# Performance work log

Measured on AMD Instinct MI355X. Metric: run time of the kernel, lower is better.

Reference implementation:

```python
import jax, jax.numpy as jnp
import numpy as np

HID = 16   # hidden_dim
K = 16     # kNN neighbors
B = 64     # graphs per batch
N_TS = 8192
N_LC = 12288


def setup_inputs() -> dict:
    key = jax.random.key(0)
    ks = jax.random.split(key, 24)

    def lin(k, fan_in, fan_out):
        w = jax.random.normal(k, (fan_in, fan_out), jnp.float32) / np.sqrt(fan_in).astype(np.float32)
        return w

    inp = {
        "x_ts": jax.random.normal(ks[0], (N_TS, 6), jnp.float32),
        "x_lc": jax.random.normal(ks[1], (N_LC, 5), jnp.float32),
        # balanced sorted graph ids -> every graph has >= K source nodes
        "batch_ts": jnp.repeat(jnp.arange(B, dtype=jnp.int32), N_TS // B),
        "batch_lc": jnp.repeat(jnp.arange(B, dtype=jnp.int32), N_LC // B),
        # ts_encode: Linear(6,16), ELU, Linear(16,16), ELU
        "ts_w1": lin(ks[2], 6, HID),  "ts_b1": jnp.zeros((HID,), jnp.float32),
        "ts_w2": lin(ks[3], HID, HID), "ts_b2": jnp.zeros((HID,), jnp.float32),
        # lc_encode: Linear(5,16), ELU, Linear(16,16), ELU
        "lc_w1": lin(ks[4], 5, HID),  "lc_b1": jnp.zeros((HID,), jnp.float32),
        "lc_w2": lin(ks[5], HID, HID), "lc_b2": jnp.zeros((HID,), jnp.float32),
        # EdgeConv nn: Linear(2*16, 16), ELU  (shared across the 3 conv calls)
        "conv_w": lin(ks[6], 2 * HID, HID), "conv_b": jnp.zeros((HID,), jnp.float32),
        # output MLP 16->64->32->8->4->1 (ELU between, none after last)
        "out_w1": lin(ks[7], HID, 64), "out_b1": jnp.zeros((64,), jnp.float32),
        "out_w2": lin(ks[8], 64, 32),  "out_b2": jnp.zeros((32,), jnp.float32),
        "out_w3": lin(ks[9], 32, 8),   "out_b3": jnp.zeros((8,), jnp.float32),
        "out_w4": lin(ks[10], 8, 4),   "out_b4": jnp.zeros((4,), jnp.float32),
        "out_w5": lin(ks[11], 4, 1),   "out_b5": jnp.zeros((1,), jnp.float32),
    }
    return inp


def _mlp2(x, w1, b1, w2, b2):
    return jax.nn.elu(jax.nn.elu(x @ w1 + b1) @ w2 + b2)


def _edge_conv(x_src, x_dst, b_src, b_dst, w, b):
    """DynamicEdgeConv: per-graph kNN of dst queries into src, message
    nn(cat[x_i, x_j - x_i]), max-aggregate over the K neighbors."""
    # squared distances [N_dst, N_src]
    d2 = (jnp.sum(x_dst * x_dst, 1)[:, None]
          - 2.0 * (x_dst @ x_src.T)
          + jnp.sum(x_src * x_src, 1)[None, :])
    d2 = jnp.where(b_dst[:, None] == b_src[None, :], d2, jnp.inf)
    _, idx = jax.lax.top_k(-d2, K)          # [N_dst, K] nearest (incl. self when src==dst)
    xj = x_src[idx]                          # [N_dst, K, H] gather
    xi = x_dst[:, None, :]                   # [N_dst, 1, H]
    msg = jnp.concatenate([jnp.broadcast_to(xi, xj.shape), xj - xi], axis=-1)
    msg = jax.nn.elu(msg @ w + b)            # [N_dst, K, H]
    return jnp.max(msg, axis=1)              # max aggregation -> [N_dst, H]


def reference(x_ts, x_lc, batch_ts, batch_lc,
              ts_w1, ts_b1, ts_w2, ts_b2,
              lc_w1, lc_b1, lc_w2, lc_b2,
              conv_w, conv_b,
              out_w1, out_b1, out_w2, out_b2, out_w3, out_b3,
              out_w4, out_b4, out_w5, out_b5):
    x_ts_enc = _mlp2(x_ts, ts_w1, ts_b1, ts_w2, ts_b2)   # [N_ts, 16]
    x_lc_enc = _mlp2(x_lc, lc_w1, lc_b1, lc_w2, lc_b2)   # [N_lc, 16]

    feats1 = _edge_conv(x_lc_enc, x_lc_enc, batch_lc, batch_lc, conv_w, conv_b)  # [N_lc,16]
    feats2 = _edge_conv(x_lc_enc, x_ts_enc, batch_lc, batch_ts, conv_w, conv_b)  # [N_ts,16]
    feats3 = _edge_conv(feats1,   feats2,   batch_lc, batch_ts, conv_w, conv_b)  # [N_ts,16]

    # avg_pool_x(batch_ts, feats3, batch_ts): per-graph mean
    sums = jax.ops.segment_sum(feats3, batch_ts, num_segments=B)
    cnts = jax.ops.segment_sum(jnp.ones((feats3.shape[0],), feats3.dtype), batch_ts, num_segments=B)
    pooled = sums / cnts[:, None]                         # [B, 16]

    h = jax.nn.elu(pooled @ out_w1 + out_b1)
    h = jax.nn.elu(h @ out_w2 + out_b2)
    h = jax.nn.elu(h @ out_w3 + out_b3)
    h = jax.nn.elu(h @ out_w4 + out_b4)
    out = h @ out_w5 + out_b5                             # [B, 1]
    batch_out = jnp.arange(B, dtype=batch_ts.dtype)
    return (out, batch_out)
```

## Files before the change

### kernel.cpp

```cpp
#include <hip/hip_runtime.h>
#include <math.h>

#define HID 16
#define KNN 16
#define NB 64
#define NTS 8192
#define NLC 12288
#define TSG 128
#define LCG 192

__device__ __forceinline__ float eluf(float x) {
    return x > 0.0f ? x : expm1f(x);
}

__device__ __forceinline__ unsigned int f2ord(float f) {
    unsigned int b = __float_as_uint(f);
    return b ^ (((int)b >> 31) | 0x80000000u);
}

__global__ __launch_bounds__(256) void encode_kernel(
    const float* __restrict__ x_ts, const float* __restrict__ x_lc,
    const float* __restrict__ ts_w1, const float* __restrict__ ts_b1,
    const float* __restrict__ ts_w2, const float* __restrict__ ts_b2,
    const float* __restrict__ lc_w1, const float* __restrict__ lc_b1,
    const float* __restrict__ lc_w2, const float* __restrict__ lc_b2,
    const float* __restrict__ cw,
    float* __restrict__ ts_enc, float* __restrict__ lc_enc,
    float* __restrict__ y_lc, float* __restrict__ n_lc,
    float* __restrict__ pooled)
{
    __shared__ float sw1[6 * HID];
    __shared__ float sw2[HID * HID];
    __shared__ float scw2[HID * HID];
    __shared__ float sb1[HID];
    __shared__ float sb2[HID];
    __shared__ float s_h[64 * 17];

    const int tid = threadIdx.x;
    const int t = blockIdx.x * 256 + tid;
    if (t < NB * HID) pooled[t] = 0.0f;

    const bool is_ts = (blockIdx.x < NTS / 64);
    const float* w1 = is_ts ? ts_w1 : lc_w1;
    const float* b1 = is_ts ? ts_b1 : lc_b1;
    const float* w2 = is_ts ? ts_w2 : lc_w2;
    const float* b2 = is_ts ? ts_b2 : lc_b2;
    const int in_dim = is_ts ? 6 : 5;

    if (tid < in_dim * HID) sw1[tid] = w1[tid];
    if (tid < HID * HID)    sw2[tid] = w2[tid];
    if (!is_ts && tid < HID * HID) scw2[tid] = cw[HID * HID + tid];
    if (tid < HID)          { sb1[tid] = b1[tid]; sb2[tid] = b2[tid]; }
    __syncthreads();

    const int q    = tid & 3;
    const int rloc = tid >> 2;
    const int row  = is_ts ? (blockIdx.x * 64 + rloc)
                           : ((blockIdx.x - 128) * 64 + rloc);
    const float* x = is_ts ? (x_ts + (size_t)row * 6) : (x_lc + (size_t)row * 5);
    float* outp    = is_ts ? (ts_enc + (size_t)row * HID) : (lc_enc + (size_t)row * HID);

    float xin[6];
    for (int k = 0; k < in_dim; ++k) xin[k] = x[k];

    #pragma unroll
    for (int jc = 0; jc < 4; ++jc) {
        const int c = 4 * q + jc;
        float s = sb1[c];
        for (int k = 0; k < in_dim; ++k) s += xin[k] * sw1[k * HID + c];
        s_h[rloc * 17 + c] = eluf(s);
    }
    __syncthreads();
    float hf[HID];
    #pragma unroll
    for (int k = 0; k < HID; ++k) hf[k] = s_h[rloc * 17 + k];

    float o4v[4];
    #pragma unroll
    for (int jc = 0; jc < 4; ++jc) {
        const int c = 4 * q + jc;
        float s = sb2[c];
        #pragma unroll
        for (int k = 0; k < HID; ++k) s += hf[k] * sw2[k * HID + c];
        o4v[jc] = eluf(s);
    }
    reinterpret_cast<float4*>(outp)[q] = make_float4(o4v[0], o4v[1], o4v[2], o4v[3]);

    if (!is_ts) {
        __syncthreads();
        #pragma unroll
        for (int jc = 0; jc < 4; ++jc) s_h[rloc * 17 + 4 * q + jc] = o4v[jc];
        __syncthreads();
        float of[HID];
        #pragma unroll
        for (int k = 0; k < HID; ++k) of[k] = s_h[rloc * 17 + k];
        float nv = 0.f;
        #pragma unroll
        for (int c = 0; c < HID; ++c) nv += of[c] * of[c];
        float y4[4];
        #pragma unroll
        for (int jc = 0; jc < 4; ++jc) {
            const int c = 4 * q + jc;
            float s = 0.f;
            #pragma unroll
            for (int k = 0; k < HID; ++k) s += of[k] * scw2[k * HID + c];
            y4[jc] = s;
        }
        reinterpret_cast<float4*>(y_lc + (size_t)row * HID)[q] =
            make_float4(y4[0], y4[1], y4[2], y4[3]);
        if (q == 0) n_lc[row] = nv;
    }
}

#define CONV_SMEM_FLOATS (LCG * HID + 2 * HID * HID + 2 * HID)
#define CONV_SMEM_BYTES  (CONV_SMEM_FLOATS * 4)

template<int NSRC, int NDST, bool POOL, bool EPI>
__device__ __forceinline__ void edgeconv_impl(
    float* __restrict__ smem, int bid,
    const float* __restrict__ src, const float* __restrict__ src_y,
    const float* __restrict__ src_n, const float* __restrict__ dst,
    const float* __restrict__ cw, const float* __restrict__ cb,
    float* __restrict__ out_feats, float* __restrict__ out_y,
    float* __restrict__ out_n, float* __restrict__ pool_out)
{
    constexpr int RPB = 8;
    constexpr int BPG = NDST / RPB;
    float* s_y    = smem;
    float* s_dw   = s_y + NSRC * HID;
    float* s_w2   = s_dw + HID * HID;
    float* s_b    = s_w2 + HID * HID;
    float* s_pool = s_b + HID;

    const int tid  = threadIdx.x;
    const int lane = tid & 63;
    const int wave = tid >> 6;
    const int g      = bid / BPG;
    const int rowblk = bid % BPG;

    if (tid < HID * HID) {
        float w1v = cw[tid];
        float w2v = cw[HID * HID + tid];
        s_dw[tid] = w1v - w2v;
        if (EPI) s_w2[tid] = w2v;
    }
    if (tid < HID) s_b[tid] = cb[tid];
    if (POOL && tid < HID) s_pool[tid] = 0.0f;
    {
        const float4* gy = reinterpret_cast<const float4*>(src_y + (size_t)(g * NSRC) * HID);
        float4* sy4 = reinterpret_cast<float4*>(s_y);
        for (int i = tid; i < NSRC * HID / 4; i += 512) sy4[i] = gy[i];
    }

    float rw[3][HID];
    float rn[3];
    #pragma unroll
    for (int k = 0; k < 3; ++k) {
        const float4* rp = reinterpret_cast<const float4*>(src + (size_t)(g * NSRC + lane + 64 * k) * HID);
        float4 a = rp[0], b = rp[1], c4 = rp[2], e = rp[3];
        rw[k][0] = a.x;  rw[k][1] = a.y;  rw[k][2]  = a.z;  rw[k][3]  = a.w;
        rw[k][4] = b.x;  rw[k][5] = b.y;  rw[k][6]  = b.z;  rw[k][7]  = b.w;
        rw[k][8] = c4.x; rw[k][9] = c4.y; rw[k][10] = c4.z; rw[k][11] = c4.w;
        rw[k][12] = e.x; rw[k][13] = e.y; rw[k][14] = e.z;  rw[k][15] = e.w;
        rn[k] = src_n[g * NSRC + lane + 64 * k];
    }

    const int drow = rowblk * RPB + wave;
    const float4* d4 = reinterpret_cast<const float4*>(dst + (size_t)(g * NDST + drow) * HID);
    float xi[HID];
    {
        float4 a = d4[0], b = d4[1], c4 = d4[2], e = d4[3];
        xi[0] = a.x;  xi[1] = a.y;  xi[2]  = a.z;  xi[3]  = a.w;
        xi[4] = b.x;  xi[5] = b.y;  xi[6]  = b.z;  xi[7]  = b.w;
        xi[8] = c4.x; xi[9] = c4.y; xi[10] = c4.z; xi[11] = c4.w;
        xi[12] = e.x; xi[13] = e.y; xi[14] = e.z;  xi[15] = e.w;
    }
    float nd = 0.f;
    #pragma unroll
    for (int c = 0; c < HID; ++c) nd += xi[c] * xi[c];

    unsigned int dk0, dk1, dk2;
    {
        unsigned int dk[3];
        #pragma unroll
        for (int k = 0; k < 3; ++k) {
            float dot = 0.f;
            #pragma unroll
            for (int c = 0; c < HID; ++c) dot += xi[c] * rw[k][c];
            dk[k] = f2ord(nd - 2.0f * dot + rn[k]);
        }
        dk0 = dk[0]; dk1 = dk[1]; dk2 = dk[2];
    }

    unsigned int p = 0;
    int k = KNN;
    for (int b = 31; b >= 0; --b) {
        unsigned int pb = p >> b;
        int cnt = __popcll(__ballot((dk0 >> b) == pb))
                + __popcll(__ballot((dk1 >> b) == pb))
                + __popcll(__ballot((dk2 >> b) == pb));
        if (k > cnt) { k -= cnt; p |= (1u << b); }
    }
    int cnt_eq = __popcll(__ballot(dk0 == p))
               + __popcll(__ballot(dk1 == p))
               + __popcll(__ballot(dk2 == p));
    unsigned int qi = 255u;
    if (cnt_eq != k) {
        qi = 0;
        int kk = k;
        const unsigned int i0 = (unsigned)lane, i1 = (unsigned)(lane + 64), i2 = (unsigned)(lane + 128);
        for (int b = 7; b >= 0; --b) {
            unsigned int qb = qi >> b;
            int cnt = __popcll(__ballot(dk0 == p && (i0 >> b) == qb))
                    + __popcll(__ballot(dk1 == p && (i1 >> b) == qb))
                    + __popcll(__ballot(dk2 == p && (i2 >> b) == qb));
            if (kk > cnt) { kk -= cnt; qi |= (1u << b); }
        }
    }
    unsigned long long m0 = __ballot(dk0 < p || (dk0 == p && (unsigned)lane <= qi));
    unsigned long long m1 = __ballot(dk1 < p || (dk1 == p && (unsigned)(lane + 64) <= qi));
    unsigned long long m2 = __ballot(dk2 < p || (dk2 == p && (unsigned)(lane + 128) <= qi));

    __syncthreads();

    const int c = lane & 15;
    float cic = s_b[c];
    #pragma unroll
    for (int r = 0; r < HID; ++r) cic += xi[r] * s_dw[r * HID + c];

    int jarr[KNN];
    #pragma unroll
    for (int i = 0; i < KNN; ++i) {
        int j;
        if (m0)      { j = __builtin_ctzll(m0);       m0 &= m0 - 1; }
        else if (m1) { j = 64 + __builtin_ctzll(m1);  m1 &= m1 - 1; }
        else         { j = 128 + __builtin_ctzll(m2); m2 &= m2 - 1; }
        jarr[i] = j;
    }
    float yv[KNN];
    #pragma unroll
    for (int i = 0; i < KNN; ++i) yv[i] = s_y[jarr[i] * HID + c];
    float ym = yv[0];
    #pragma unroll
    for (int i = 1; i < KNN; ++i) ym = fmaxf(ym, yv[i]);

    const float f = eluf(cic + ym);

    if (POOL) {
        if (lane < HID) atomicAdd(&s_pool[c], f);
        __syncthreads();
        if (tid < HID) atomicAdd(&pool_out[g * HID + tid], s_pool[tid]);
    } else {
        const int grow = g * NDST + drow;
        if (lane < HID) out_feats[(size_t)grow * HID + c] = f;
        if (EPI) {
            float yvv = 0.f, nv = 0.f;
            #pragma unroll
            for (int r = 0; r < HID; ++r) {
                float fr = __shfl(f, r, 64);
                yvv += fr * s_w2[r * HID + c];
                nv += fr * fr;
            }
            if (lane < HID) out_y[(size_t)grow * HID + c] = yvv;
            if (lane == 0)  out_n[grow] = nv;
        }
    }
}

#define C1_BLOCKS (NB * (LCG / 8))
#define C2_BLOCKS (NB * (TSG / 8))
__global__ __launch_bounds__(512) void edgeconv12_kernel(
    const float* __restrict__ lc_enc, const float* __restrict__ y_lc,
    const float* __restrict__ n_lc, const float* __restrict__ ts_enc,
    const float* __restrict__ cw, const float* __restrict__ cb,
    float* __restrict__ feats1, float* __restrict__ y_f1, float* __restrict__ n_f1,
    float* __restrict__ feats2)
{
    extern __shared__ float smem[];
    if (blockIdx.x < C1_BLOCKS)
        edgeconv_impl<LCG, LCG, false, true>(smem, blockIdx.x, lc_enc, y_lc, n_lc,
                                             lc_enc, cw, cb, feats1, y_f1, n_f1, nullptr);
    else
        edgeconv_impl<LCG, TSG, false, false>(smem, blockIdx.x - C1_BLOCKS, lc_enc, y_lc, n_lc,
                                              ts_enc, cw, cb, feats2, nullptr, nullptr, nullptr);
}

__global__ __launch_bounds__(512) void edgeconv3_kernel(
    const float* __restrict__ feats1, const float* __restrict__ y_f1,
    const float* __restrict__ n_f1, const float* __restrict__ feats2,
    const float* __restrict__ cw, const float* __restrict__ cb,
    float* __restrict__ pooled)
{
    extern __shared__ float smem[];
    edgeconv_impl<LCG, TSG, true, false>(smem, blockIdx.x, feats1, y_f1, n_f1,
                                         feats2, cw, cb, nullptr, nullptr, nullptr, pooled);
}

__global__ __launch_bounds__(64) void head_kernel(
    const float* __restrict__ pooled,
    const float* __restrict__ w1, const float* __restrict__ b1,
    const float* __restrict__ w2, const float* __restrict__ b2,
    const float* __restrict__ w3, const float* __restrict__ b3,
    const float* __restrict__ w4, const float* __restrict__ b4,
    const float* __restrict__ w5, const float* __restrict__ b5,
    float* __restrict__ out)
{
    const int g = blockIdx.x;
    const int lane = threadIdx.x;
    __shared__ float sp[HID];
    __shared__ float sh1[64];
    __shared__ float sh2[32];
    __shared__ float sh3[8];
    __shared__ float sh4[4];

    if (lane < HID) sp[lane] = pooled[g * HID + lane] * (1.0f / (float)TSG);
    __syncthreads();

    {
        float s = b1[lane];
        #pragma unroll
        for (int r = 0; r < HID; ++r) s += sp[r] * w1[r * 64 + lane];
        sh1[lane] = eluf(s);
    }
    __syncthreads();
    if (lane < 32) {
        float s = b2[lane];
        #pragma unroll
        for (int r = 0; r < 64; ++r) s += sh1[r] * w2[r * 32 + lane];
        sh2[lane] = eluf(s);
    }
    __syncthreads();
    if (lane < 8) {
        float s = b3[lane];
        #pragma unroll
        for (int r = 0; r < 32; ++r) s += sh2[r] * w3[r * 8 + lane];
        sh3[lane] = eluf(s);
    }
    __syncthreads();
    if (lane < 4) {
        float s = b4[lane];
        #pragma unroll
        for (int r = 0; r < 8; ++r) s += sh3[r] * w4[r * 4 + lane];
        sh4[lane] = eluf(s);
    }
    __syncthreads();
    if (lane == 0) {
        float s = b5[0];
        #pragma unroll
        for (int r = 0; r < 4; ++r) s += sh4[r] * w5[r];
        out[g] = s;
        out[NB + g] = (float)g;
    }
}

extern "C" void kernel_launch(void* const* d_in, const int* in_sizes, int n_in,
                              void* d_out, int out_size, void* d_ws, size_t ws_size,
                              hipStream_t stream) {
    const float* x_ts  = (const float*)d_in[0];
    const float* x_lc  = (const float*)d_in[1];
    const float* ts_w1 = (const float*)d_in[4];
    const float* ts_b1 = (const float*)d_in[5];
    const float* ts_w2 = (const float*)d_in[6];
    const float* ts_b2 = (const float*)d_in[7];
    const float* lc_w1 = (const float*)d_in[8];
    const float* lc_b1 = (const float*)d_in[9];
    const float* lc_w2 = (const float*)d_in[10];
    const float* lc_b2 = (const float*)d_in[11];
    const float* cw    = (const float*)d_in[12];
    const float* cb    = (const float*)d_in[13];
    const float* ow1   = (const float*)d_in[14];
    const float* ob1   = (const float*)d_in[15];
    const float* ow2   = (const float*)d_in[16];
    const float* ob2   = (const float*)d_in[17];
    const float* ow3   = (const float*)d_in[18];
    const float* ob3   = (const float*)d_in[19];
    const float* ow4   = (const float*)d_in[20];
    const float* ob4   = (const float*)d_in[21];
    const float* ow5   = (const float*)d_in[22];
    const float* ob5   = (const float*)d_in[23];
    float* out = (float*)d_out;

    float* ws = (float*)d_ws;
    float* ts_enc = ws;
    float* lc_enc = ws + 131072;
    float* feats1 = ws + 327680;
    float* feats2 = ws + 524288;
    float* pooled = ws + 655360;
    float* y_lc   = ws + 656384;
    float* n_lc   = ws + 852992;
    float* y_f1   = ws + 865280;
    float* n_f1   = ws + 1061888;

    encode_kernel<<<(NTS + NLC) / 64, 256, 0, stream>>>(
        x_ts, x_lc, ts_w1, ts_b1, ts_w2, ts_b2, lc_w1, lc_b1, lc_w2, lc_b2,
        cw, ts_enc, lc_enc, y_lc, n_lc, pooled);

    edgeconv12_kernel<<<C1_BLOCKS + C2_BLOCKS, 512, CONV_SMEM_BYTES, stream>>>(
        lc_enc, y_lc, n_lc, ts_enc, cw, cb, feats1, y_f1, n_f1, feats2);

    edgeconv3_kernel<<<C2_BLOCKS, 512, CONV_SMEM_BYTES, stream>>>(
        feats1, y_f1, n_f1, feats2, cw, cb, pooled);

    head_kernel<<<NB, 64, 0, stream>>>(
        pooled, ow1, ob1, ow2, ob2, ow3, ob3, ow4, ob4, ow5, ob5, out);
}
```

Measured before the change: 156.6 us.

## Drop shared-memory staging in edgeconv, use wave-independent blocks and 16-bit radix select

Each edge-conv block no longer stages the per-graph y table and the weight matrices in shared memory. Every wave now handles one destination row on its own, reading source rows and y values straight from global memory (cached). The kNN radix select now runs over the upper 16 bits first and only refines the lower 16 bits when there are ties, which cuts the usual number of ballot rounds. The W1-W2 difference is precomputed once in the encode kernel, and the pooling now does one global atomic per wave instead of a shared-memory reduction. These changes remove block-wide syncs and LDS traffic and should raise occupancy, at the cost of redundant global and L2 reads and more global atomics.

Result: slower. 163.6 us (+4.5%).

```diff
diff --git a/kernel.cpp b/kernel.cpp
--- a/kernel.cpp
+++ b/kernel.cpp
@@ -27,7 +27,7 @@
     const float* __restrict__ cw,
     float* __restrict__ ts_enc, float* __restrict__ lc_enc,
     float* __restrict__ y_lc, float* __restrict__ n_lc,
-    float* __restrict__ pooled)
+    float* __restrict__ pooled, float* __restrict__ dw_ws)
 {
     __shared__ float sw1[6 * HID];
     __shared__ float sw2[HID * HID];
@@ -39,6 +39,7 @@
     const int tid = threadIdx.x;
     const int t = blockIdx.x * 256 + tid;
     if (t < NB * HID) pooled[t] = 0.0f;
+    if (blockIdx.x == 0) dw_ws[tid] = cw[tid] - cw[HID * HID + tid];
 
     const bool is_ts = (blockIdx.x < NTS / 64);
     const float* w1 = is_ts ? ts_w1 : lc_w1;
@@ -112,60 +113,20 @@
     }
 }
 
-#define CONV_SMEM_FLOATS (LCG * HID + 2 * HID * HID + 2 * HID)
-#define CONV_SMEM_BYTES  (CONV_SMEM_FLOATS * 4)
-
-template<int NSRC, int NDST, bool POOL, bool EPI>
-__device__ __forceinline__ void edgeconv_impl(
-    float* __restrict__ smem, int bid,
+template<int NSRC, int NDST, int MODE>
+__device__ __forceinline__ void edgeconv_wave(
+    int wid,
     const float* __restrict__ src, const float* __restrict__ src_y,
     const float* __restrict__ src_n, const float* __restrict__ dst,
-    const float* __restrict__ cw, const float* __restrict__ cb,
+    const float* __restrict__ dw, const float* __restrict__ w2,
+    const float* __restrict__ cb,
     float* __restrict__ out_feats, float* __restrict__ out_y,
     float* __restrict__ out_n, float* __restrict__ pool_out)
 {
-    constexpr int RPB = 8;
-    constexpr int BPG = NDST / RPB;
-    float* s_y    = smem;
-    float* s_dw   = s_y + NSRC * HID;
-    float* s_w2   = s_dw + HID * HID;
-    float* s_b    = s_w2 + HID * HID;
-    float* s_pool = s_b + HID;
-
-    const int tid  = threadIdx.x;
-    const int lane = tid & 63;
-    const int wave = tid >> 6;
-    const int g      = bid / BPG;
-    const int rowblk = bid % BPG;
-
-    if (tid < HID * HID) {
-        float w1v = cw[tid];
-        float w2v = cw[HID * HID + tid];
-        s_dw[tid] = w1v - w2v;
-        if (EPI) s_w2[tid] = w2v;
-    }
-    if (tid < HID) s_b[tid] = cb[tid];
-    if (POOL && tid < HID) s_pool[tid] = 0.0f;
-    {
-        const float4* gy = reinterpret_cast<const float4*>(src_y + (size_t)(g * NSRC) * HID);
-        float4* sy4 = reinterpret_cast<float4*>(s_y);
-        for (int i = tid; i < NSRC * HID / 4; i += 512) sy4[i] = gy[i];
-    }
-
-    float rw[3][HID];
-    float rn[3];
-    #pragma unroll
-    for (int k = 0; k < 3; ++k) {
-        const float4* rp = reinterpret_cast<const float4*>(src + (size_t)(g * NSRC + lane + 64 * k) * HID);
-        float4 a = rp[0], b = rp[1], c4 = rp[2], e = rp[3];
-        rw[k][0] = a.x;  rw[k][1] = a.y;  rw[k][2]  = a.z;  rw[k][3]  = a.w;
-        rw[k][4] = b.x;  rw[k][5] = b.y;  rw[k][6]  = b.z;  rw[k][7]  = b.w;
-        rw[k][8] = c4.x; rw[k][9] = c4.y; rw[k][10] = c4.z; rw[k][11] = c4.w;
-        rw[k][12] = e.x; rw[k][13] = e.y; rw[k][14] = e.z;  rw[k][15] = e.w;
-        rn[k] = src_n[g * NSRC + lane + 64 * k];
-    }
-
-    const int drow = rowblk * RPB + wave;
+    const int lane = threadIdx.x & 63;
+    const int g    = wid / NDST;
+    const int drow = wid % NDST;
+
     const float4* d4 = reinterpret_cast<const float4*>(dst + (size_t)(g * NDST + drow) * HID);
     float xi[HID];
     {
@@ -179,86 +140,105 @@
     #pragma unroll
     for (int c = 0; c < HID; ++c) nd += xi[c] * xi[c];
 
-    unsigned int dk0, dk1, dk2;
-    {
-        unsigned int dk[3];
-        #pragma unroll
-        for (int k = 0; k < 3; ++k) {
-            float dot = 0.f;
-            #pragma unroll
-            for (int c = 0; c < HID; ++c) dot += xi[c] * rw[k][c];
-            dk[k] = f2ord(nd - 2.0f * dot + rn[k]);
-        }
-        dk0 = dk[0]; dk1 = dk[1]; dk2 = dk[2];
-    }
-
+    const float* r0 = src + (size_t)(g * NSRC + lane) * HID;
+    const float* r1 = r0 + 64 * HID;
+    const float* r2 = r0 + 128 * HID;
+    float dot0 = 0.f, dot1 = 0.f, dot2 = 0.f;
+    #pragma unroll
+    for (int q = 0; q < 4; ++q) {
+        float4 a0 = reinterpret_cast<const float4*>(r0)[q];
+        float4 a1 = reinterpret_cast<const float4*>(r1)[q];
+        float4 a2 = reinterpret_cast<const float4*>(r2)[q];
+        dot0 += xi[4*q+0]*a0.x; dot0 += xi[4*q+1]*a0.y; dot0 += xi[4*q+2]*a0.z; dot0 += xi[4*q+3]*a0.w;
+        dot1 += xi[4*q+0]*a1.x; dot1 += xi[4*q+1]*a1.y; dot1 += xi[4*q+2]*a1.z; dot1 += xi[4*q+3]*a1.w;
+        dot2 += xi[4*q+0]*a2.x; dot2 += xi[4*q+1]*a2.y; dot2 += xi[4*q+2]*a2.z; dot2 += xi[4*q+3]*a2.w;
+    }
+    const float* np_ = src_n + g * NSRC + lane;
+    const unsigned int dk0 = f2ord(nd - 2.0f * dot0 + np_[0]);
+    const unsigned int dk1 = f2ord(nd - 2.0f * dot1 + np_[64]);
+    const unsigned int dk2 = f2ord(nd - 2.0f * dot2 + np_[128]);
+
+    const unsigned int h0 = dk0 >> 16, h1 = dk1 >> 16, h2 = dk2 >> 16;
     unsigned int p = 0;
     int k = KNN;
-    for (int b = 31; b >= 0; --b) {
+    for (int b = 15; b >= 0; --b) {
         unsigned int pb = p >> b;
-        int cnt = __popcll(__ballot((dk0 >> b) == pb))
-                + __popcll(__ballot((dk1 >> b) == pb))
-                + __popcll(__ballot((dk2 >> b) == pb));
+        int cnt = __popcll(__ballot((h0 >> b) == pb))
+                + __popcll(__ballot((h1 >> b) == pb))
+                + __popcll(__ballot((h2 >> b) == pb));
         if (k > cnt) { k -= cnt; p |= (1u << b); }
     }
-    int cnt_eq = __popcll(__ballot(dk0 == p))
-               + __popcll(__ballot(dk1 == p))
-               + __popcll(__ballot(dk2 == p));
+    int cnt_eq = __popcll(__ballot(h0 == p))
+               + __popcll(__ballot(h1 == p))
+               + __popcll(__ballot(h2 == p));
+    unsigned int p2 = 0xFFFFu;
     unsigned int qi = 255u;
     if (cnt_eq != k) {
-        qi = 0;
-        int kk = k;
-        const unsigned int i0 = (unsigned)lane, i1 = (unsigned)(lane + 64), i2 = (unsigned)(lane + 128);
-        for (int b = 7; b >= 0; --b) {
-            unsigned int qb = qi >> b;
-            int cnt = __popcll(__ballot(dk0 == p && (i0 >> b) == qb))
-                    + __popcll(__ballot(dk1 == p && (i1 >> b) == qb))
-                    + __popcll(__ballot(dk2 == p && (i2 >> b) == qb));
-            if (kk > cnt) { kk -= cnt; qi |= (1u << b); }
+        const bool e0 = (h0 == p), e1 = (h1 == p), e2 = (h2 == p);
+        const unsigned int l0 = dk0 & 0xFFFFu, l1 = dk1 & 0xFFFFu, l2 = dk2 & 0xFFFFu;
+        p2 = 0;
+        for (int b = 15; b >= 0; --b) {
+            unsigned int pb = p2 >> b;
+            int cnt = __popcll(__ballot(e0 && (l0 >> b) == pb))
+                    + __popcll(__ballot(e1 && (l1 >> b) == pb))
+                    + __popcll(__ballot(e2 && (l2 >> b) == pb));
+            if (k > cnt) { k -= cnt; p2 |= (1u << b); }
         }
-    }
-    unsigned long long m0 = __ballot(dk0 < p || (dk0 == p && (unsigned)lane <= qi));
-    unsigned long long m1 = __ballot(dk1 < p || (dk1 == p && (unsigned)(lane + 64) <= qi));
-    unsigned long long m2 = __ballot(dk2 < p || (dk2 == p && (unsigned)(lane + 128) <= qi));
-
-    __syncthreads();
+        int cnt2 = __popcll(__ballot(e0 && l0 == p2))
+                 + __popcll(__ballot(e1 && l1 == p2))
+                 + __popcll(__ballot(e2 && l2 == p2));
+        if (cnt2 != k) {
+            const bool f0 = e0 && (l0 == p2), f1 = e1 && (l1 == p2), f2 = e2 && (l2 == p2);
+            qi = 0;
+            for (int b = 7; b >= 0; --b) {
+                unsigned int qb = qi >> b;
+                int cnt = __popcll(__ballot(f0 && ((unsigned)lane >> b) == qb))
+                        + __popcll(__ballot(f1 && ((unsigned)(lane + 64) >> b) == qb))
+                        + __popcll(__ballot(f2 && ((unsigned)(lane + 128) >> b) == qb));
+                if (k > cnt) { k -= cnt; qi |= (1u << b); }
+            }
+        }
+    }
+    const unsigned int P = (p << 16) | p2;
+    unsigned long long m0 = __ballot(dk0 < P || (dk0 == P && (unsigned)lane <= qi));
+    unsigned long long m1 = __ballot(dk1 < P || (dk1 == P && (unsigned)(lane + 64) <= qi));
+    unsigned long long m2 = __ballot(dk2 < P || (dk2 == P && (unsigned)(lane + 128) <= qi));
 
     const int c = lane & 15;
-    float cic = s_b[c];
-    #pragma unroll
-    for (int r = 0; r < HID; ++r) cic += xi[r] * s_dw[r * HID + c];
-
-    int jarr[KNN];
+    float cic = cb[c];
+    #pragma unroll
+    for (int r = 0; r < HID; ++r) cic += xi[r] * dw[r * HID + c];
+
+    int js[KNN];
     #pragma unroll
     for (int i = 0; i < KNN; ++i) {
         int j;
         if (m0)      { j = __builtin_ctzll(m0);       m0 &= m0 - 1; }
         else if (m1) { j = 64 + __builtin_ctzll(m1);  m1 &= m1 - 1; }
         else         { j = 128 + __builtin_ctzll(m2); m2 &= m2 - 1; }
-        jarr[i] = j;
-    }
+        js[i] = j;
+    }
+    const float* ybase = src_y + (size_t)g * NSRC * HID;
     float yv[KNN];
     #pragma unroll
-    for (int i = 0; i < KNN; ++i) yv[i] = s_y[jarr[i] * HID + c];
+    for (int i = 0; i < KNN; ++i) yv[i] = ybase[js[i] * HID + c];
     float ym = yv[0];
     #pragma unroll
     for (int i = 1; i < KNN; ++i) ym = fmaxf(ym, yv[i]);
 
     const float f = eluf(cic + ym);
 
-    if (POOL) {
-        if (lane < HID) atomicAdd(&s_pool[c], f);
-        __syncthreads();
-        if (tid < HID) atomicAdd(&pool_out[g * HID + tid], s_pool[tid]);
+    if (MODE == 2) {
+        if (lane < HID) atomicAdd(&pool_out[g * HID + c], f);
     } else {
         const int grow = g * NDST + drow;
         if (lane < HID) out_feats[(size_t)grow * HID + c] = f;
-        if (EPI) {
+        if (MODE == 1) {
             float yvv = 0.f, nv = 0.f;
             #pragma unroll
             for (int r = 0; r < HID; ++r) {
                 float fr = __shfl(f, r, 64);
-                yvv += fr * s_w2[r * HID + c];
+                yvv += fr * w2[r * HID + c];
                 nv += fr * fr;
             }
             if (lane < HID) out_y[(size_t)grow * HID + c] = yvv;
@@ -267,33 +247,34 @@
     }
 }
 
-#define C1_BLOCKS (NB * (LCG / 8))
-#define C2_BLOCKS (NB * (TSG / 8))
-__global__ __launch_bounds__(512) void edgeconv12_kernel(
+#define C1_WAVES (NB * LCG)
+#define C2_WAVES (NB * TSG)
+__global__ __launch_bounds__(256) void edgeconv12_kernel(
     const float* __restrict__ lc_enc, const float* __restrict__ y_lc,
     const float* __restrict__ n_lc, const float* __restrict__ ts_enc,
-    const float* __restrict__ cw, const float* __restrict__ cb,
+    const float* __restrict__ dw, const float* __restrict__ cw,
+    const float* __restrict__ cb,
     float* __restrict__ feats1, float* __restrict__ y_f1, float* __restrict__ n_f1,
     float* __restrict__ feats2)
 {
-    extern __shared__ float smem[];
-    if (blockIdx.x < C1_BLOCKS)
-        edgeconv_impl<LCG, LCG, false, true>(smem, blockIdx.x, lc_enc, y_lc, n_lc,
-                                             lc_enc, cw, cb, feats1, y_f1, n_f1, nullptr);
+    const int wid = blockIdx.x * 4 + (threadIdx.x >> 6);
+    if (wid < C1_WAVES)
+        edgeconv_wave<LCG, LCG, 1>(wid, lc_enc, y_lc, n_lc, lc_enc,
+                                   dw, cw + HID * HID, cb, feats1, y_f1, n_f1, nullptr);
     else
-        edgeconv_impl<LCG, TSG, false, false>(smem, blockIdx.x - C1_BLOCKS, lc_enc, y_lc, n_lc,
-                                              ts_enc, cw, cb, feats2, nullptr, nullptr, nullptr);
-}
-
-__global__ __launch_bounds__(512) void edgeconv3_kernel(
+        edgeconv_wave<LCG, TSG, 0>(wid - C1_WAVES, lc_enc, y_lc, n_lc, ts_enc,
+                                   dw, nullptr, cb, feats2, nullptr, nullptr, nullptr);
+}
+
+__global__ __launch_bounds__(256) void edgeconv3_kernel(
     const float* __restrict__ feats1, const float* __restrict__ y_f1,
     const float* __restrict__ n_f1, const float* __restrict__ feats2,
-    const float* __restrict__ cw, const float* __restrict__ cb,
+    const float* __restrict__ dw, const float* __restrict__ cb,
     float* __restrict__ pooled)
 {
-    extern __shared__ float smem[];
-    edgeconv_impl<LCG, TSG, true, false>(smem, blockIdx.x, feats1, y_f1, n_f1,
-                                         feats2, cw, cb, nullptr, nullptr, nullptr, pooled);
+    const int wid = blockIdx.x * 4 + (threadIdx.x >> 6);
+    edgeconv_wave<LCG, TSG, 2>(wid, feats1, y_f1, n_f1, feats2,
+                               dw, nullptr, cb, nullptr, nullptr, nullptr, pooled);
 }
 
 __global__ __launch_bounds__(64) void head_kernel(
@@ -390,16 +371,17 @@
     float* n_lc   = ws + 852992;
     float* y_f1   = ws + 865280;
     float* n_f1   = ws + 1061888;
+    float* dw_ws  = ws + 1074176;
 
     encode_kernel<<<(NTS + NLC) / 64, 256, 0, stream>>>(
         x_ts, x_lc, ts_w1, ts_b1, ts_w2, ts_b2, lc_w1, lc_b1, lc_w2, lc_b2,
-        cw, ts_enc, lc_enc, y_lc, n_lc, pooled);
-
-    edgeconv12_kernel<<<C1_BLOCKS + C2_BLOCKS, 512, CONV_SMEM_BYTES, stream>>>(
-        lc_enc, y_lc, n_lc, ts_enc, cw, cb, feats1, y_f1, n_f1, feats2);
-
-    edgeconv3_kernel<<<C2_BLOCKS, 512, CONV_SMEM_BYTES, stream>>>(
-        feats1, y_f1, n_f1, feats2, cw, cb, pooled);
+        cw, ts_enc, lc_enc, y_lc, n_lc, pooled, dw_ws);
+
+    edgeconv12_kernel<<<(C1_WAVES + C2_WAVES) / 4, 256, 0, stream>>>(
+        lc_enc, y_lc, n_lc, ts_enc, dw_ws, cw, cb, feats1, y_f1, n_f1, feats2);
+
+    edgeconv3_kernel<<<C2_WAVES / 4, 256, 0, stream>>>(
+        feats1, y_f1, n_f1, feats2, dw_ws, cb, pooled);
 
     head_kernel<<<NB, 64, 0, stream>>>(
         pooled, ow1, ob1, ow2, ob2, ow3, ob3, ow4, ob4, ow5, ob5, out);
```
